# Kernel optimization log

Measured on AMD Instinct MI355X. Metric: run time of the kernel, lower is better.

Reference implementation:

```python
import jax, jax.numpy as jnp
import numpy as np

B, S, D, V = 4, 512, 512, 32000
GAMMA = 0.5
EPS = 1e-12  # torch F.normalize clamp_min eps


def _l2norm(x, axis):
    n = jnp.sqrt(jnp.sum(x * x, axis=axis, keepdims=True))
    return x / jnp.maximum(n, EPS)


def setup_inputs() -> dict:
    key = jax.random.key(0)
    k1, k2, k3 = jax.random.split(key, 3)
    preds = jax.random.normal(k1, (B, D, S), dtype=jnp.float32)
    emb_weight = jax.random.normal(k2, (V, D), dtype=jnp.float32)
    target = jax.random.randint(k3, (B, S), 0, V, dtype=jnp.int64)
    return {"preds": preds, "emb_weight": emb_weight, "target": target, "pad_id": 0}


def reference(preds, emb_weight, target, pad_id):
    # preds: [B, D, S] -> [B, S, D], L2-normalized over D
    out_norm = _l2norm(jnp.transpose(preds, (0, 2, 1)), axis=2)
    voc_norm = _l2norm(emb_weight, axis=1)          # [V, D]
    tgt_emb = emb_weight[target]                     # [B, S, D] (raw lookup, not normalized)
    mask = target != pad_id                          # [B, S]

    cos_out_voc = jnp.einsum('bsd,vd->bsv', out_norm, voc_norm)  # [B, S, V]
    tgt_voc = jnp.einsum('bsd,vd->bsv', tgt_emb, voc_norm)       # [B, S, V]

    jmax = jnp.argmax(cos_out_voc - tgt_voc, axis=2)             # [B, S]
    cos_target = jnp.take_along_axis(cos_out_voc, target[..., None], axis=2)[..., 0]
    max_cos_voc = jnp.take_along_axis(cos_out_voc, jmax[..., None], axis=2)[..., 0]

    diff = jnp.maximum(GAMMA + max_cos_voc - cos_target, 0.0)    # [B, S]
    denom = jnp.sum(mask).astype(diff.dtype)
    return jnp.sum(jnp.where(mask, diff, 0.0)) / denom
```

## Files before the change

### kernel.cpp

```cpp
#include <hip/hip_runtime.h>
#include <math.h>


#define Bb 4
#define Ss 512
#define Dd 512
#define Vv 32000
#define ROWS (Bb * Ss)
#define NTILE_M (ROWS / 128)
#define NTILE_N (Vv / 128)
#define VOC_PER_BLK 16
#define VOC_BLOCKS (Vv / VOC_PER_BLK)
#define COL_BLOCKS 256
#define MARGIN 0.5f

typedef __attribute__((ext_vector_type(4))) float f32x4;

__device__ __forceinline__ float waveReduceSum(float x) {
#pragma unroll
  for (int m = 32; m >= 1; m >>= 1) x += __shfl_xor(x, m, 64);
  return x;
}

__device__ __forceinline__ float waveReduceMax(float x) {
#pragma unroll
  for (int m = 32; m >= 1; m >>= 1) x = fmaxf(x, __shfl_xor(x, m, 64));
  return x;
}

__device__ __forceinline__ unsigned char f2e4m3(float f) {
  int p = __builtin_amdgcn_cvt_pk_fp8_f32(f, f, 0, false);
  return (unsigned char)(p & 0xff);
}

__device__ __forceinline__ void async_ld16(const void* g, void* l) {
  __builtin_amdgcn_global_load_lds((const __attribute__((address_space(1))) void*)g,
                                   (__attribute__((address_space(3))) void*)l, 16, 0, 0);
}

__global__ __launch_bounds__(256) void prep_all(
    const float* __restrict__ preds, const float* __restrict__ emb,
    const int* __restrict__ target,
    float* __restrict__ o_rows, unsigned char* __restrict__ u8,
    float* __restrict__ cos_tgt, unsigned char* __restrict__ e8,
    float* __restrict__ inv_norm) {
  int tid = threadIdx.x;
  int wave = tid >> 6, lane = tid & 63;
  if (blockIdx.x < VOC_BLOCKS) {
    int vbase = blockIdx.x * VOC_PER_BLK + wave * 4;
    float4 xa[4], xb[4];
#pragma unroll
    for (int r = 0; r < 4; ++r) {
      const float* e = emb + (size_t)(vbase + r) * Dd + lane * 8;
      xa[r] = *(const float4*)e;
      xb[r] = *(const float4*)(e + 4);
    }
    float ss[4];
#pragma unroll
    for (int r = 0; r < 4; ++r)
      ss[r] = xa[r].x * xa[r].x + xa[r].y * xa[r].y + xa[r].z * xa[r].z +
              xa[r].w * xa[r].w + xb[r].x * xb[r].x + xb[r].y * xb[r].y +
              xb[r].z * xb[r].z + xb[r].w * xb[r].w;
#pragma unroll
    for (int m = 32; m >= 1; m >>= 1) {
#pragma unroll
      for (int r = 0; r < 4; ++r) ss[r] += __shfl_xor(ss[r], m, 64);
    }
#pragma unroll
    for (int r = 0; r < 4; ++r) {
      float inv = 1.0f / fmaxf(sqrtf(ss[r]), 1e-12f);
      int lo = __builtin_amdgcn_cvt_pk_fp8_f32(xa[r].x * inv, xa[r].y * inv, 0, false);
      lo = __builtin_amdgcn_cvt_pk_fp8_f32(xa[r].z * inv, xa[r].w * inv, lo, true);
      int hi = __builtin_amdgcn_cvt_pk_fp8_f32(xb[r].x * inv, xb[r].y * inv, 0, false);
      hi = __builtin_amdgcn_cvt_pk_fp8_f32(xb[r].z * inv, xb[r].w * inv, hi, true);
      *(int2*)(e8 + (size_t)(vbase + r) * Dd + lane * 8) = make_int2(lo, hi);
      if (lane == 0) inv_norm[vbase + r] = inv;
    }
  } else {
    __shared__ float st[Dd * 9];
    int cb = blockIdx.x - VOC_BLOCKS;
    int b = cb >> 6, sg = cb & 63;
    int s0 = sg * 8;
    const float* pb = preds + (size_t)b * Dd * Ss + s0;
    {
      int d = tid;
      float4 a0 = *(const float4*)(pb + (size_t)d * Ss);
      float4 a1 = *(const float4*)(pb + (size_t)d * Ss + 4);
      st[d * 9 + 0] = a0.x; st[d * 9 + 1] = a0.y;
      st[d * 9 + 2] = a0.z; st[d * 9 + 3] = a0.w;
      st[d * 9 + 4] = a1.x; st[d * 9 + 5] = a1.y;
      st[d * 9 + 6] = a1.z; st[d * 9 + 7] = a1.w;
      d = tid + 256;
      float4 b0 = *(const float4*)(pb + (size_t)d * Ss);
      float4 b1 = *(const float4*)(pb + (size_t)d * Ss + 4);
      st[d * 9 + 0] = b0.x; st[d * 9 + 1] = b0.y;
      st[d * 9 + 2] = b0.z; st[d * 9 + 3] = b0.w;
      st[d * 9 + 4] = b1.x; st[d * 9 + 5] = b1.y;
      st[d * 9 + 6] = b1.z; st[d * 9 + 7] = b1.w;
    }
    __syncthreads();
#pragma unroll
    for (int u = 0; u < 2; ++u) {
      int sj = wave * 2 + u;
      int row = b * Ss + s0 + sj;
      float ov[8];
      float ssq = 0.f;
#pragma unroll
      for (int k = 0; k < 8; ++k) {
        float x = st[(lane + 64 * k) * 9 + sj];
        ov[k] = x;
        ssq += x * x;
      }
      ssq = waveReduceSum(ssq);
      float inv = 1.0f / fmaxf(sqrtf(ssq), 1e-12f);
      int t = target[row];
      const float* et = emb + (size_t)t * Dd;
      float ss2 = 0.f, dt = 0.f;
#pragma unroll
      for (int k = 0; k < 8; ++k) {
        int d = lane + 64 * k;
        float o = ov[k] * inv;
        float e = et[d];
        o_rows[(size_t)row * Dd + d] = o;
        u8[(size_t)row * Dd + d] = f2e4m3(o - e);
        ss2 += e * e;
        dt += o * e;
      }
      ss2 = waveReduceSum(ss2);
      dt = waveReduceSum(dt);
      if (lane == 0) cos_tgt[row] = dt * (1.0f / fmaxf(sqrtf(ss2), 1e-12f));
    }
  }
}

__global__ __launch_bounds__(256, 4) void gemm_argmax(
    const unsigned char* __restrict__ u8, const unsigned char* __restrict__ e8,
    float* __restrict__ part_s, int* __restrict__ part_i) {
  __shared__ unsigned char sA[128 * 128];
  __shared__ unsigned char sB[128 * 128];
  int bid = blockIdx.x;
  int g = (bid & 7) * 500 + (bid >> 3);
  int tm = g & 15, tn = g >> 4;
  int tid = threadIdx.x;
  int w = tid >> 6, lane = tid & 63;
  int wm = w >> 1, wn = w & 1;

  int srow = w * 8 + (lane >> 3);
  int schunk = (lane & 7) ^ ((lane >> 3) & 7);
  const unsigned char* gA = u8 + (size_t)(tm * 128 + srow) * Dd + schunk * 16;
  const unsigned char* gB = e8 + (size_t)(tn * 128 + srow) * Dd + schunk * 16;

  int fr = lane & 15;
  int q = lane >> 4;
  int qh = q >> 1, ql = (q & 1) * 8;
  int flow = fr & 7;

  f32x4 acc[4][4];
  f32x4 z = {0.f, 0.f, 0.f, 0.f};
#pragma unroll
  for (int mi = 0; mi < 4; ++mi)
#pragma unroll
    for (int ni = 0; ni < 4; ++ni) acc[mi][ni] = z;

  for (int kk = 0; kk < 4; ++kk) {
    __syncthreads();
    {
      const unsigned char* ga = gA + kk * 128;
      const unsigned char* gb = gB + kk * 128;
#pragma unroll
      for (int i = 0; i < 4; ++i) {
        async_ld16(ga + (size_t)(i * 32) * Dd, &sA[(w * 8 + i * 32) * 128]);
        async_ld16(gb + (size_t)(i * 32) * Dd, &sB[(w * 8 + i * 32) * 128]);
      }
    }
    __syncthreads();
#pragma unroll
    for (int kc = 0; kc < 4; ++kc) {
      int off = ((2 * kc + qh) ^ flow) * 16 + ql;
      long af[4], bg[4];
#pragma unroll
      for (int mi = 0; mi < 4; ++mi)
        af[mi] = *(const long*)(sA + (wm * 64 + mi * 16 + fr) * 128 + off);
#pragma unroll
      for (int ni = 0; ni < 4; ++ni)
        bg[ni] = *(const long*)(sB + (wn * 64 + ni * 16 + fr) * 128 + off);
#pragma unroll
      for (int mi = 0; mi < 4; ++mi)
#pragma unroll
        for (int ni = 0; ni < 4; ++ni)
          acc[mi][ni] = __builtin_amdgcn_mfma_f32_16x16x32_fp8_fp8(af[mi], bg[ni], acc[mi][ni], 0, 0, 0);
    }
  }

  float bs[4][4];
  int bc[4][4];
  int col0 = tn * 128 + wn * 64 + (lane & 15);
#pragma unroll
  for (int mi = 0; mi < 4; ++mi) {
#pragma unroll
    for (int j = 0; j < 4; ++j) { bs[mi][j] = acc[mi][0][j]; bc[mi][j] = col0; }
#pragma unroll
    for (int ni = 1; ni < 4; ++ni) {
      int c = col0 + ni * 16;
#pragma unroll
      for (int j = 0; j < 4; ++j) {
        float v = acc[mi][ni][j];
        if (v > bs[mi][j]) { bs[mi][j] = v; bc[mi][j] = c; }
      }
    }
  }
#pragma unroll
  for (int m = 1; m < 16; m <<= 1) {
#pragma unroll
    for (int mi = 0; mi < 4; ++mi)
#pragma unroll
      for (int j = 0; j < 4; ++j) {
        float os = __shfl_xor(bs[mi][j], m, 64);
        int oc = __shfl_xor(bc[mi][j], m, 64);
        if (os > bs[mi][j] || (os == bs[mi][j] && oc < bc[mi][j])) {
          bs[mi][j] = os;
          bc[mi][j] = oc;
        }
      }
  }
  __syncthreads();
  float* sEs = (float*)sA;
  int* sEc = (int*)sA + 256;
  if ((lane & 15) == 0) {
    int qq = lane >> 4;
#pragma unroll
    for (int mi = 0; mi < 4; ++mi)
#pragma unroll
      for (int j = 0; j < 4; ++j) {
        int rloc = wm * 64 + mi * 16 + qq * 4 + j;
        sEs[wn * 128 + rloc] = bs[mi][j];
        sEc[wn * 128 + rloc] = bc[mi][j];
      }
  }
  __syncthreads();
  if (tid < 128) {
    float s0 = sEs[tid], s1 = sEs[128 + tid];
    int c0 = sEc[tid], c1 = sEc[128 + tid];
    if (s1 > s0 || (s1 == s0 && c1 < c0)) { s0 = s1; c0 = c1; }
    part_s[(size_t)(tm * 128 + tid) * 256 + tn] = s0;
    part_i[(size_t)(tm * 128 + tid) * 256 + tn] = c0;
  }
}

__global__ __launch_bounds__(256) void row_final(
    const float* __restrict__ o_rows, const float* __restrict__ emb,
    const float* __restrict__ inv_norm, const float* __restrict__ cos_tgt,
    const int* __restrict__ target, const int* __restrict__ pad_id,
    const float* __restrict__ part_s, const int* __restrict__ part_i,
    float* __restrict__ diffs) {
  int row = blockIdx.x;
  int tid = threadIdx.x;
  int w = tid >> 6, lane = tid & 63;
  __shared__ float sMax[4];
  __shared__ int sCand[256];
  __shared__ int sCnt;
  __shared__ float sBs[4], sBp[4];
  __shared__ int sBc[4];
  float v = (tid < NTILE_N) ? part_s[(size_t)row * 256 + tid] : -INFINITY;
  float wmax = waveReduceMax(v);
  if (lane == 0) sMax[w] = wmax;
  if (tid == 0) sCnt = 0;
  __syncthreads();
  float thr = fmaxf(fmaxf(sMax[0], sMax[1]), fmaxf(sMax[2], sMax[3])) - MARGIN;
  if (tid < NTILE_N && v >= thr) {
    int idx = atomicAdd(&sCnt, 1);
    sCand[idx] = part_i[(size_t)row * 256 + tid];
  }
  __syncthreads();
  int n = sCnt;
  int tgt = target[row];
  const float* o = o_rows + (size_t)row * Dd;
  const float* et = emb + (size_t)tgt * Dd;
  float4 oa = *(const float4*)(o + lane * 8);
  float4 ob = *(const float4*)(o + lane * 8 + 4);
  float4 ta = *(const float4*)(et + lane * 8);
  float4 tb = *(const float4*)(et + lane * 8 + 4);
  float bscore = -INFINITY, bpo = 0.f;
  int bcol = 0x7fffffff;
  for (int i = w; i < n; i += 4) {
    int c = sCand[i];
    const float* ec = emb + (size_t)c * Dd;
    float4 ea = *(const float4*)(ec + lane * 8);
    float4 eb = *(const float4*)(ec + lane * 8 + 4);
    float po = oa.x * ea.x + oa.y * ea.y + oa.z * ea.z + oa.w * ea.w +
               ob.x * eb.x + ob.y * eb.y + ob.z * eb.z + ob.w * eb.w;
    float pt = ta.x * ea.x + ta.y * ea.y + ta.z * ea.z + ta.w * ea.w +
               tb.x * eb.x + tb.y * eb.y + tb.z * eb.z + tb.w * eb.w;
    po = waveReduceSum(po);
    pt = waveReduceSum(pt);
    float sc = (po - pt) * inv_norm[c];
    if (sc > bscore || (sc == bscore && c < bcol)) {
      bscore = sc;
      bcol = c;
      bpo = po;
    }
  }
  if (lane == 0) { sBs[w] = bscore; sBc[w] = bcol; sBp[w] = bpo; }
  __syncthreads();
  if (tid == 0) {
    float s = sBs[0], p = sBp[0];
    int c = sBc[0];
#pragma unroll
    for (int i = 1; i < 4; ++i)
      if (sBs[i] > s || (sBs[i] == s && sBc[i] < c)) { s = sBs[i]; c = sBc[i]; p = sBp[i]; }
    float cmax = p * inv_norm[c];
    float df = fmaxf(0.5f + cmax - cos_tgt[row], 0.0f);
    diffs[row] = (tgt != pad_id[0]) ? df : 0.0f;
  }
}

__global__ __launch_bounds__(256) void reduce_final(
    const float* __restrict__ diffs, const int* __restrict__ target,
    const int* __restrict__ pad_id, float* __restrict__ out) {
  int tid = threadIdx.x;
  int pid = pad_id[0];
  float s = 0.f, c = 0.f;
  for (int i = tid; i < ROWS; i += 256) {
    s += diffs[i];
    c += (target[i] != pid) ? 1.0f : 0.0f;
  }
  s = waveReduceSum(s);
  c = waveReduceSum(c);
  __shared__ float rs[4], rc[4];
  int wave = tid >> 6, lane = tid & 63;
  if (lane == 0) { rs[wave] = s; rc[wave] = c; }
  __syncthreads();
  if (tid == 0) out[0] = (rs[0] + rs[1] + rs[2] + rs[3]) / (rc[0] + rc[1] + rc[2] + rc[3]);
}

extern "C" void kernel_launch(void* const* d_in, const int* in_sizes, int n_in,
                              void* d_out, int out_size, void* d_ws, size_t ws_size,
                              hipStream_t stream) {
  const float* preds = (const float*)d_in[0];
  const float* emb = (const float*)d_in[1];
  const int* target = (const int*)d_in[2];
  const int* pad_id = (const int*)d_in[3];
  char* ws = (char*)d_ws;
  float* o_rows = (float*)ws;
  unsigned char* u8 = (unsigned char*)(ws + 4194304);
  unsigned char* e8 = (unsigned char*)(ws + 5242880);
  float* inv_norm = (float*)(ws + 21626880);
  float* cos_tgt = (float*)(ws + 21754880);
  float* part_s = (float*)(ws + 21763072);
  int* part_i = (int*)(ws + 23860224);
  float* diffs = (float*)(ws + 25957376);

  prep_all<<<VOC_BLOCKS + COL_BLOCKS, 256, 0, stream>>>(preds, emb, target, o_rows, u8,
                                                        cos_tgt, e8, inv_norm);
  gemm_argmax<<<NTILE_M * NTILE_N, 256, 0, stream>>>(u8, e8, part_s, part_i);
  row_final<<<ROWS, 256, 0, stream>>>(o_rows, emb, inv_norm, cos_tgt, target,
                                      pad_id, part_s, part_i, diffs);
  reduce_final<<<1, 256, 0, stream>>>(diffs, target, pad_id, (float*)d_out);
}
```

Before: 192.4 us.

## Use 8-wave GEMM blocks with 256-byte K stages and 32x64 warp tiles

The fp8 GEMM+argmax kernel moves from 4 waves to 8 waves per 128x128 tile. Each wave now owns a 32x64 sub-tile instead of 64x64, and the K loop loads 256-byte slices in two stages instead of 128-byte slices in four. This halves the sync count and per-wave accumulator registers to raise occupancy and latency hiding. The cost is doubled LDS per block (64KB) and less operand reuse per wave. The XOR swizzle now uses only the low 8 chunks, while each row holds 16 chunks per stage.

```diff
diff --git a/kernel.cpp b/kernel.cpp
--- a/kernel.cpp
+++ b/kernel.cpp
@@ -133,11 +133,11 @@
   }
 }
 
-__global__ __launch_bounds__(256, 4) void gemm_argmax(
+__global__ __launch_bounds__(512, 4) void gemm_argmax(
     const unsigned char* __restrict__ u8, const unsigned char* __restrict__ e8,
     float* __restrict__ part_s, int* __restrict__ part_i) {
-  __shared__ unsigned char sA[128 * 128];
-  __shared__ unsigned char sB[128 * 128];
+  __shared__ unsigned char sA[128 * 256];
+  __shared__ unsigned char sB[128 * 256];
   int bid = blockIdx.x;
   int g = (bid & 7) * 500 + (bid >> 3);
   int tm = g & 15, tn = g >> 4;
@@ -145,58 +145,52 @@
   int w = tid >> 6, lane = tid & 63;
   int wm = w >> 1, wn = w & 1;
 
-  int srow = w * 8 + (lane >> 3);
-  int schunk = (lane & 7) ^ ((lane >> 3) & 7);
-  const unsigned char* gA = u8 + (size_t)(tm * 128 + srow) * Dd + schunk * 16;
-  const unsigned char* gB = e8 + (size_t)(tn * 128 + srow) * Dd + schunk * 16;
+  int rin = lane >> 4;
+  int cch = lane & 15;
 
   int fr = lane & 15;
   int q = lane >> 4;
   int qh = q >> 1, ql = (q & 1) * 8;
   int flow = fr & 7;
 
-  f32x4 acc[4][4];
+  f32x4 acc[2][4];
   f32x4 z = {0.f, 0.f, 0.f, 0.f};
 #pragma unroll
-  for (int mi = 0; mi < 4; ++mi)
+  for (int mi = 0; mi < 2; ++mi)
 #pragma unroll
     for (int ni = 0; ni < 4; ++ni) acc[mi][ni] = z;
 
-  for (int kk = 0; kk < 4; ++kk) {
+  for (int ks = 0; ks < 2; ++ks) {
+    if (ks) __syncthreads();
+#pragma unroll
+    for (int i = 0; i < 4; ++i) {
+      int rloc = w * 16 + i * 4 + rin;
+      int ch = cch ^ (rloc & 7);
+      async_ld16(u8 + (size_t)(tm * 128 + rloc) * Dd + ks * 256 + ch * 16,
+                 &sA[(w * 16 + i * 4) * 256]);
+      async_ld16(e8 + (size_t)(tn * 128 + rloc) * Dd + ks * 256 + ch * 16,
+                 &sB[(w * 16 + i * 4) * 256]);
+    }
     __syncthreads();
-    {
-      const unsigned char* ga = gA + kk * 128;
-      const unsigned char* gb = gB + kk * 128;
-#pragma unroll
-      for (int i = 0; i < 4; ++i) {
-        async_ld16(ga + (size_t)(i * 32) * Dd, &sA[(w * 8 + i * 32) * 128]);
-        async_ld16(gb + (size_t)(i * 32) * Dd, &sB[(w * 8 + i * 32) * 128]);
-      }
-    }
-    __syncthreads();
-#pragma unroll
-    for (int kc = 0; kc < 4; ++kc) {
+#pragma unroll
+    for (int kc = 0; kc < 8; ++kc) {
       int off = ((2 * kc + qh) ^ flow) * 16 + ql;
-      long af[4], bg[4];
-#pragma unroll
-      for (int mi = 0; mi < 4; ++mi)
-        af[mi] = *(const long*)(sA + (wm * 64 + mi * 16 + fr) * 128 + off);
-#pragma unroll
-      for (int ni = 0; ni < 4; ++ni)
-        bg[ni] = *(const long*)(sB + (wn * 64 + ni * 16 + fr) * 128 + off);
-#pragma unroll
-      for (int mi = 0; mi < 4; ++mi)
-#pragma unroll
-        for (int ni = 0; ni < 4; ++ni)
-          acc[mi][ni] = __builtin_amdgcn_mfma_f32_16x16x32_fp8_fp8(af[mi], bg[ni], acc[mi][ni], 0, 0, 0);
-    }
-  }
-
-  float bs[4][4];
-  int bc[4][4];
+      long af0 = *(const long*)(sA + (wm * 32 + fr) * 256 + off);
+      long af1 = *(const long*)(sA + (wm * 32 + 16 + fr) * 256 + off);
+#pragma unroll
+      for (int ni = 0; ni < 4; ++ni) {
+        long b = *(const long*)(sB + (wn * 64 + ni * 16 + fr) * 256 + off);
+        acc[0][ni] = __builtin_amdgcn_mfma_f32_16x16x32_fp8_fp8(af0, b, acc[0][ni], 0, 0, 0);
+        acc[1][ni] = __builtin_amdgcn_mfma_f32_16x16x32_fp8_fp8(af1, b, acc[1][ni], 0, 0, 0);
+      }
+    }
+  }
+
+  float bs[2][4];
+  int bc[2][4];
   int col0 = tn * 128 + wn * 64 + (lane & 15);
 #pragma unroll
-  for (int mi = 0; mi < 4; ++mi) {
+  for (int mi = 0; mi < 2; ++mi) {
 #pragma unroll
     for (int j = 0; j < 4; ++j) { bs[mi][j] = acc[mi][0][j]; bc[mi][j] = col0; }
 #pragma unroll
@@ -212,7 +206,7 @@
 #pragma unroll
   for (int m = 1; m < 16; m <<= 1) {
 #pragma unroll
-    for (int mi = 0; mi < 4; ++mi)
+    for (int mi = 0; mi < 2; ++mi)
 #pragma unroll
       for (int j = 0; j < 4; ++j) {
         float os = __shfl_xor(bs[mi][j], m, 64);
@@ -229,10 +223,10 @@
   if ((lane & 15) == 0) {
     int qq = lane >> 4;
 #pragma unroll
-    for (int mi = 0; mi < 4; ++mi)
+    for (int mi = 0; mi < 2; ++mi)
 #pragma unroll
       for (int j = 0; j < 4; ++j) {
-        int rloc = wm * 64 + mi * 16 + qq * 4 + j;
+        int rloc = wm * 32 + mi * 16 + qq * 4 + j;
         sEs[wn * 128 + rloc] = bs[mi][j];
         sEc[wn * 128 + rloc] = bc[mi][j];
       }
@@ -352,7 +346,7 @@
 
   prep_all<<<VOC_BLOCKS + COL_BLOCKS, 256, 0, stream>>>(preds, emb, target, o_rows, u8,
                                                         cos_tgt, e8, inv_norm);
-  gemm_argmax<<<NTILE_M * NTILE_N, 256, 0, stream>>>(u8, e8, part_s, part_i);
+  gemm_argmax<<<NTILE_M * NTILE_N, 512, 0, stream>>>(u8, e8, part_s, part_i);
   row_final<<<ROWS, 256, 0, stream>>>(o_rows, emb, inv_norm, cos_tgt, target,
                                       pad_id, part_s, part_i, diffs);
   reduce_final<<<1, 256, 0, stream>>>(diffs, target, pad_id, (float*)d_out);
```

Measured after the change: 208.2 us. 1.08x slower.
